# Optimization experiments

Hardware: AMD Instinct MI355X
Metric: run time of the kernel (lower is better)

Reference implementation:

```python
import jax, jax.numpy as jnp
import numpy as np

TEMP = 0.7
B, V, C, H, W = 4, 2, 128, 32, 32  # V=2 views


def setup_inputs() -> dict:
    key = jax.random.key(0)
    k1, k2 = jax.random.split(key)
    feats = jax.random.normal(k1, (B, V, C, H, W), dtype=jnp.float32)
    # 'cos_dst' in the original implies L2-normalized embeddings along C
    feats = feats / jnp.linalg.norm(feats, axis=2, keepdims=True)
    labels = jax.random.randint(k2, (B, V, H, W), 0, 4, dtype=jnp.int32)
    return {"features": feats, "labels": labels}


def reference(features, labels):
    # split views on dim=1 and concat on batch (as in torch forward)
    f = jnp.concatenate([features[:, 0], features[:, 1]], axis=0)  # [2B, C, H, W]
    lab = jnp.concatenate([labels[:, 0], labels[:, 1]], axis=0)     # [2B, H, W]
    c = f.shape[1]
    # flatten pixels in (b, i, j) order -> [N, C]
    F_ = jnp.transpose(f, (0, 2, 3, 1)).reshape(-1, c)
    L_ = lab.reshape(-1)                                            # [N]
    # pairwise similarities: the triple loop's per-anchor 1x1 conv, batched
    S = jnp.einsum('nc,mc->nm', F_, F_) / TEMP                      # [N, N]
    diag = jnp.diagonal(S)                                          # self-contrast per anchor
    same = (L_[None, :] == L_[:, None]).astype(S.dtype)             # positives mask (incl. self)
    num = jnp.sum(same * S, axis=1) - diag
    den = jnp.sum(jnp.exp(S), axis=1) - jnp.exp(diag)
    cnt = jnp.sum(same, axis=1) - 1.0                               # mask.sum() - 1
    valid = (L_ != 0)                                               # x_label == 1 (label 0) skipped
    cnt_safe = jnp.where(valid, cnt, 1.0)
    loss_a = jnp.where(valid, jnp.log(den) - num / cnt_safe, 0.0)
    n_valid = jnp.sum(valid.astype(S.dtype))
    return jnp.where(n_valid > 0, jnp.sum(loss_a) / jnp.maximum(n_valid, 1.0), 0.0)
```

## Files before the change

### kernel.cpp

```cpp
#include <hip/hip_runtime.h>

#define TEMP 0.7f
#define LOG2E 1.4426950408889634f
#define LN2 0.6931471805599453f
#define NPIX 8192
#define CDIM 128
#define NCHUNK 64
#define FSCALE 1.4356161f
#define EXPDIAG 4.1727352f

typedef __bf16 v8bf __attribute__((ext_vector_type(8)));
typedef float f32x4 __attribute__((ext_vector_type(4)));

#define OFF_G      0
#define OFF_COUNTS 512
#define OFF_ACC    516
#define OFF_DONE   517
#define OFF_ZERON  520
#define OFF_PART   1024
#define OFF_SWF    (1024 + NCHUNK * NPIX)

__global__ __launch_bounds__(256) void k0_zero(float* __restrict__ w) {
    const int i = blockIdx.x * 256 + threadIdx.x;
    if (i < OFF_ZERON) w[i] = 0.0f;
}

__global__ __launch_bounds__(256) void k1_build(
    const float* __restrict__ feats, const int* __restrict__ labels,
    v8bf* __restrict__ swf, float* __restrict__ G, int* __restrict__ counts)
{
    __shared__ float lds[128][33];
    __shared__ int lab_l[32];
    __shared__ float cs[2][4][128];

    const int t = threadIdx.x;
    const int bp = blockIdx.x >> 5;
    const int pc = blockIdx.x & 31;
    const int b = bp & 3, v = bp >> 2;
    const int bv = b * 2 + v;
    const int p0 = pc * 32;
    const int nbase = bp * 1024 + p0;

    const float* src = feats + (size_t)bv * CDIM * 1024 + p0;
    const int px = t & 31, c8 = t >> 5;
#pragma unroll
    for (int i = 0; i < 16; i++) {
        const int c = i * 8 + c8;
        lds[c][px] = src[c * 1024 + px];
    }
    if (t < 32) {
        const int lab = labels[bv * 1024 + p0 + t];
        lab_l[t] = lab;
#pragma unroll
        for (int k = 0; k < 4; k++) {
            unsigned long long m = __ballot(lab == k);
            if (t == 0) atomicAdd(&counts[k], (int)__popcll(m));
        }
    }
    __syncthreads();

    {
        const int cw = t & 127, h = t >> 7;
        float s0 = 0.f, s1 = 0.f, s2 = 0.f, s3 = 0.f;
#pragma unroll
        for (int i = 0; i < 16; i++) {
            const int nl = h * 16 + i;
            const int lab = lab_l[nl];
            const float f = lds[cw][nl];
            s0 += (lab == 0) ? f : 0.f;
            s1 += (lab == 1) ? f : 0.f;
            s2 += (lab == 2) ? f : 0.f;
            s3 += (lab == 3) ? f : 0.f;
        }
        cs[h][0][cw] = s0; cs[h][1][cw] = s1;
        cs[h][2][cw] = s2; cs[h][3][cw] = s3;
    }
    __syncthreads();
    if (t < 128) {
#pragma unroll
        for (int k = 0; k < 4; k++)
            atomicAdd(&G[k * CDIM + t], cs[0][k][t] + cs[1][k][t]);
    }

#pragma unroll
    for (int i2 = 0; i2 < 2; i2++) {
        const int slot = i2 * 256 + t;
        const int f = slot >> 6, l = slot & 63;
        const int ctl = f >> 2, kk = f & 3;
        const int q = l >> 4, r = l & 15;
        const int nl = ctl * 16 + r;
        const int c0 = kk * 32 + q * 8;
        v8bf val;
#pragma unroll
        for (int j = 0; j < 8; j++) val[j] = (__bf16)(lds[c0 + j][nl] * FSCALE);
        const int ctg = (nbase >> 4) + ctl;
        swf[(ctg * 4 + kk) * 64 + l] = val;
    }
}

__device__ __forceinline__ void stage_tile(const v8bf* swf, __bf16* ldsbase,
                                           int ct, int wave, int lane)
{
    const char* g = (const char*)swf + ((size_t)ct << 12) + (wave << 10) + (lane << 4);
    char* l = (char*)ldsbase + (wave << 10);
    __builtin_amdgcn_global_load_lds(
        (__attribute__((address_space(1))) void*)(char*)g,
        (__attribute__((address_space(3))) void*)l, 16, 0, 0);
}

__global__ __launch_bounds__(256, 2) void k3_gemm_expsum(
    const v8bf* __restrict__ swf, float* __restrict__ part)
{
    __shared__ __align__(16) __bf16 bbuf[8][2048];
    const int t = threadIdx.x;
    const int lane = t & 63;
    const int wave = t >> 6;
    const int rowblk = blockIdx.x & 31;
    const int colchunk = blockIdx.x >> 5;
    const int rowbase = rowblk * 256 + wave * 64;
    const int rt0 = rowbase >> 4;
    const int ct0 = colchunk * 8;

#pragma unroll
    for (int j = 0; j < 8; j++)
        stage_tile(swf, &bbuf[j][0], ct0 + j, wave, lane);

    v8bf a[4][4];
#pragma unroll
    for (int tt = 0; tt < 4; tt++)
#pragma unroll
        for (int kk = 0; kk < 4; kk++)
            a[tt][kk] = swf[((rt0 + tt) * 4 + kk) * 64 + lane];

    float rs[4][4];
#pragma unroll
    for (int tt = 0; tt < 4; tt++)
#pragma unroll
        for (int r = 0; r < 4; r++) rs[tt][r] = 0.f;

    __syncthreads();

#pragma unroll 2
    for (int it = 0; it < 8; ++it) {
        const v8bf* bb = (const v8bf*)&bbuf[it][0];
        const v8bf b0 = bb[lane];
        const v8bf b1 = bb[64 + lane];
        const v8bf b2 = bb[128 + lane];
        const v8bf b3 = bb[192 + lane];
#pragma unroll
        for (int tt = 0; tt < 4; tt++) {
            f32x4 acc = {0.f, 0.f, 0.f, 0.f};
            acc = __builtin_amdgcn_mfma_f32_16x16x32_bf16(a[tt][0], b0, acc, 0, 0, 0);
            acc = __builtin_amdgcn_mfma_f32_16x16x32_bf16(a[tt][1], b1, acc, 0, 0, 0);
            acc = __builtin_amdgcn_mfma_f32_16x16x32_bf16(a[tt][2], b2, acc, 0, 0, 0);
            acc = __builtin_amdgcn_mfma_f32_16x16x32_bf16(a[tt][3], b3, acc, 0, 0, 0);
#pragma unroll
            for (int r = 0; r < 4; r++)
                rs[tt][r] += __builtin_amdgcn_exp2f(acc[r]);
        }
    }

#pragma unroll
    for (int m = 1; m < 16; m <<= 1)
#pragma unroll
        for (int tt = 0; tt < 4; tt++)
#pragma unroll
            for (int r = 0; r < 4; r++)
                rs[tt][r] += __shfl_xor(rs[tt][r], m, 64);

    if ((lane & 15) == 0) {
        const int g = lane >> 4;
        float* dst = part + (size_t)colchunk * NPIX + rowbase;
#pragma unroll
        for (int tt = 0; tt < 4; tt++)
#pragma unroll
            for (int r = 0; r < 4; r++)
                dst[tt * 16 + g * 4 + r] = rs[tt][r];
    }
}

__global__ __launch_bounds__(256) void k4_loss(
    const float* __restrict__ feats, const int* __restrict__ labels,
    const float* __restrict__ G, const int* __restrict__ counts,
    const float* __restrict__ part, float* __restrict__ acc,
    int* __restrict__ done, float* __restrict__ out)
{
    __shared__ float pd[4][64];
    __shared__ float pq[4][64];
    const int t = threadIdx.x, lane = t & 63, w = t >> 6;
    const int n0 = blockIdx.x * 64;
    const int bp = n0 >> 10, p0 = n0 & 1023;
    const int bv = ((bp & 3) << 1) + (bp >> 2);
    const int p = p0 + lane;
    const int lab = labels[(bv << 10) + p];

    const float* src = feats + (((size_t)bv * CDIM + w * 32) << 10) + p;
    const float* g0p = G + w * 32;
    float dot = 0.f;
#pragma unroll 8
    for (int c = 0; c < 32; ++c) {
        const float f = src[(size_t)c << 10];
        const float g0 = g0p[c], g1 = g0p[CDIM + c];
        const float g2 = g0p[2 * CDIM + c], g3 = g0p[3 * CDIM + c];
        const float g = (lab == 1) ? g1 : (lab == 2) ? g2 : (lab == 3) ? g3 : g0;
        dot += f * g;
    }
    pd[w][lane] = dot;

    float ps = 0.f;
#pragma unroll 8
    for (int j = 0; j < 16; ++j)
        ps += part[(size_t)(w * 16 + j) * NPIX + n0 + lane];
    pq[w][lane] = ps;
    __syncthreads();

    if (w == 0) {
        const float den = pq[0][lane] + pq[1][lane] + pq[2][lane] + pq[3][lane]
                        - EXPDIAG;
        const float d = pd[0][lane] + pd[1][lane] + pd[2][lane] + pd[3][lane];
        float loss = 0.f;
        if (lab != 0) {
            const float num = (d - 1.0f) * (1.0f / TEMP);
            const float cnt = (float)(counts[lab] - 1);
            loss = __builtin_amdgcn_logf(den) * LN2 - num / cnt;
        }
#pragma unroll
        for (int m = 1; m < 64; m <<= 1) loss += __shfl_xor(loss, m, 64);
        if (lane == 0) {
            atomicAdd(acc, loss);
            __threadfence();
            const int old = atomicAdd(done, 1);
            if (old == 127) {
                const float tot = atomicAdd(acc, 0.0f);
                const int nv = NPIX - counts[0];
                out[0] = (nv > 0) ? tot / (float)nv : 0.0f;
            }
        }
    }
}

extern "C" void kernel_launch(void* const* d_in, const int* in_sizes, int n_in,
                              void* d_out, int out_size, void* d_ws, size_t ws_size,
                              hipStream_t stream) {
    const float* feats = (const float*)d_in[0];
    const int* labels = (const int*)d_in[1];
    float* out = (float*)d_out;
    float* W = (float*)d_ws;

    float* G      = W + OFF_G;
    int*   counts = (int*)(W + OFF_COUNTS);
    float* acc    = W + OFF_ACC;
    int*   done   = (int*)(W + OFF_DONE);
    float* part   = W + OFF_PART;
    v8bf*  swf    = (v8bf*)(W + OFF_SWF);

    k0_zero<<<3, 256, 0, stream>>>(W);
    k1_build<<<256, 256, 0, stream>>>(feats, labels, swf, G, counts);
    k3_gemm_expsum<<<32 * NCHUNK, 256, 0, stream>>>(swf, part);
    k4_loss<<<128, 256, 0, stream>>>(feats, labels, G, counts, part, acc, done, out);
}
```

Baseline: 55.39 us.

## Exploit similarity-matrix symmetry by computing only upper-triangular tiles

The GEMM+exp kernel now launches one block per upper-triangular 128x128 tile pair (2080 tiles) instead of covering the full matrix. Each off-diagonal block writes its row sums, and also reduces column sums of exp(S) through shared memory into the transposed partial slot. This roughly halves the MFMA and exp work, at the cost of extra shuffles, a shared-memory reduction and a serial loop to decode the tile index. The build kernel is also widened to 512 threads per block.

```diff
diff --git a/kernel.cpp b/kernel.cpp
--- a/kernel.cpp
+++ b/kernel.cpp
@@ -25,13 +25,13 @@
     if (i < OFF_ZERON) w[i] = 0.0f;
 }
 
-__global__ __launch_bounds__(256) void k1_build(
+__global__ __launch_bounds__(512) void k1_build(
     const float* __restrict__ feats, const int* __restrict__ labels,
     v8bf* __restrict__ swf, float* __restrict__ G, int* __restrict__ counts)
 {
     __shared__ float lds[128][33];
     __shared__ int lab_l[32];
-    __shared__ float cs[2][4][128];
+    __shared__ float cs[4][4][128];
 
     const int t = threadIdx.x;
     const int bp = blockIdx.x >> 5;
@@ -42,10 +42,10 @@
     const int nbase = bp * 1024 + p0;
 
     const float* src = feats + (size_t)bv * CDIM * 1024 + p0;
-    const int px = t & 31, c8 = t >> 5;
-#pragma unroll
-    for (int i = 0; i < 16; i++) {
-        const int c = i * 8 + c8;
+    const int px = t & 31, c16 = t >> 5;
+#pragma unroll
+    for (int i = 0; i < 8; i++) {
+        const int c = i * 16 + c16;
         lds[c][px] = src[c * 1024 + px];
     }
     if (t < 32) {
@@ -63,8 +63,8 @@
         const int cw = t & 127, h = t >> 7;
         float s0 = 0.f, s1 = 0.f, s2 = 0.f, s3 = 0.f;
 #pragma unroll
-        for (int i = 0; i < 16; i++) {
-            const int nl = h * 16 + i;
+        for (int i = 0; i < 8; i++) {
+            const int nl = h * 8 + i;
             const int lab = lab_l[nl];
             const float f = lds[cw][nl];
             s0 += (lab == 0) ? f : 0.f;
@@ -79,13 +79,12 @@
     if (t < 128) {
 #pragma unroll
         for (int k = 0; k < 4; k++)
-            atomicAdd(&G[k * CDIM + t], cs[0][k][t] + cs[1][k][t]);
-    }
-
-#pragma unroll
-    for (int i2 = 0; i2 < 2; i2++) {
-        const int slot = i2 * 256 + t;
-        const int f = slot >> 6, l = slot & 63;
+            atomicAdd(&G[k * CDIM + t],
+                      cs[0][k][t] + cs[1][k][t] + cs[2][k][t] + cs[3][k][t]);
+    }
+
+    {
+        const int f = t >> 6, l = t & 63;
         const int ctl = f >> 2, kk = f & 3;
         const int q = l >> 4, r = l & 15;
         const int nl = ctl * 16 + r;
@@ -108,33 +107,37 @@
         (__attribute__((address_space(3))) void*)l, 16, 0, 0);
 }
 
-__global__ __launch_bounds__(256, 2) void k3_gemm_expsum(
+__global__ __launch_bounds__(256, 4) void k3_gemm_expsum(
     const v8bf* __restrict__ swf, float* __restrict__ part)
 {
     __shared__ __align__(16) __bf16 bbuf[8][2048];
+    __shared__ float wcs[4][128];
     const int t = threadIdx.x;
     const int lane = t & 63;
     const int wave = t >> 6;
-    const int rowblk = blockIdx.x & 31;
-    const int colchunk = blockIdx.x >> 5;
-    const int rowbase = rowblk * 256 + wave * 64;
-    const int rt0 = rowbase >> 4;
-    const int ct0 = colchunk * 8;
+
+    int rem = blockIdx.x, bi = 0;
+    while (rem >= 64 - bi) { rem -= 64 - bi; bi++; }
+    const int bj = bi + rem;
+    const bool offdiag = (bj != bi);
+
+    const int rt0 = bi * 8 + wave * 2;
+    const int ct0 = bj * 8;
 
 #pragma unroll
     for (int j = 0; j < 8; j++)
         stage_tile(swf, &bbuf[j][0], ct0 + j, wave, lane);
 
-    v8bf a[4][4];
-#pragma unroll
-    for (int tt = 0; tt < 4; tt++)
+    v8bf a[2][4];
+#pragma unroll
+    for (int tt = 0; tt < 2; tt++)
 #pragma unroll
         for (int kk = 0; kk < 4; kk++)
             a[tt][kk] = swf[((rt0 + tt) * 4 + kk) * 64 + lane];
 
-    float rs[4][4];
-#pragma unroll
-    for (int tt = 0; tt < 4; tt++)
+    float rs[2][4];
+#pragma unroll
+    for (int tt = 0; tt < 2; tt++)
 #pragma unroll
         for (int r = 0; r < 4; r++) rs[tt][r] = 0.f;
 
@@ -147,35 +150,50 @@
         const v8bf b1 = bb[64 + lane];
         const v8bf b2 = bb[128 + lane];
         const v8bf b3 = bb[192 + lane];
-#pragma unroll
-        for (int tt = 0; tt < 4; tt++) {
+        float cc = 0.f;
+#pragma unroll
+        for (int tt = 0; tt < 2; tt++) {
             f32x4 acc = {0.f, 0.f, 0.f, 0.f};
             acc = __builtin_amdgcn_mfma_f32_16x16x32_bf16(a[tt][0], b0, acc, 0, 0, 0);
             acc = __builtin_amdgcn_mfma_f32_16x16x32_bf16(a[tt][1], b1, acc, 0, 0, 0);
             acc = __builtin_amdgcn_mfma_f32_16x16x32_bf16(a[tt][2], b2, acc, 0, 0, 0);
             acc = __builtin_amdgcn_mfma_f32_16x16x32_bf16(a[tt][3], b3, acc, 0, 0, 0);
 #pragma unroll
-            for (int r = 0; r < 4; r++)
-                rs[tt][r] += __builtin_amdgcn_exp2f(acc[r]);
-        }
+            for (int r = 0; r < 4; r++) {
+                const float e = __builtin_amdgcn_exp2f(acc[r]);
+                rs[tt][r] += e;
+                cc += e;
+            }
+        }
+        cc += __shfl_xor(cc, 16, 64);
+        cc += __shfl_xor(cc, 32, 64);
+        if (lane < 16) wcs[wave][it * 16 + lane] = cc;
     }
 
 #pragma unroll
     for (int m = 1; m < 16; m <<= 1)
 #pragma unroll
-        for (int tt = 0; tt < 4; tt++)
+        for (int tt = 0; tt < 2; tt++)
 #pragma unroll
             for (int r = 0; r < 4; r++)
                 rs[tt][r] += __shfl_xor(rs[tt][r], m, 64);
 
     if ((lane & 15) == 0) {
         const int g = lane >> 4;
-        float* dst = part + (size_t)colchunk * NPIX + rowbase;
-#pragma unroll
-        for (int tt = 0; tt < 4; tt++)
+        float* dst = part + (size_t)bj * NPIX + bi * 128 + wave * 32;
+#pragma unroll
+        for (int tt = 0; tt < 2; tt++)
 #pragma unroll
             for (int r = 0; r < 4; r++)
                 dst[tt * 16 + g * 4 + r] = rs[tt][r];
+    }
+
+    if (offdiag) {
+        __syncthreads();
+        if (t < 128) {
+            const float s = wcs[0][t] + wcs[1][t] + wcs[2][t] + wcs[3][t];
+            part[(size_t)bi * NPIX + bj * 128 + t] = s;
+        }
     }
 }
 
@@ -255,7 +273,7 @@
     v8bf*  swf    = (v8bf*)(W + OFF_SWF);
 
     k0_zero<<<3, 256, 0, stream>>>(W);
-    k1_build<<<256, 256, 0, stream>>>(feats, labels, swf, G, counts);
-    k3_gemm_expsum<<<32 * NCHUNK, 256, 0, stream>>>(swf, part);
+    k1_build<<<256, 512, 0, stream>>>(feats, labels, swf, G, counts);
+    k3_gemm_expsum<<<2080, 256, 0, stream>>>(swf, part);
     k4_loss<<<128, 256, 0, stream>>>(feats, labels, G, counts, part, acc, done, out);
 }
```

After: 52.75 us. 1.05x faster.
